# Performance work log

Measured on AMD Instinct MI355X. Metric: run time of the kernel, lower is better.

The kernel has to match this reference:

```python
import jax, jax.numpy as jnp
import numpy as np

KH = KW = 3  # fixed: distortion() generates a 9-tap (3x3) offset grid


def make_offset(h, w, dilation=1.0, skydome=True):
    """Faithful numpy port of DistortionConvLayer.distortion -> [1,h,w,9,2] (last dim = [x_off, y_off])."""
    pi = np.pi
    unit_w = 2.0 * pi / w
    unit_h = pi / (2.0 * h) if skydome else pi / h
    rho = np.tan(unit_w) * dilation
    v = np.array([0.0, 1.0, 0.0])
    r_grid = np.array([[1, -1], [1, 0], [1, 1], [0, -1], [0, 0], [0, 1], [-1, -1], [-1, 0], [-1, 1]], dtype=np.float64)
    xc = int(w * 0.5)
    theta = (xc - 0.5 * w) * unit_w
    y = np.arange(h, dtype=np.float64)
    phi = (h - y) * unit_h if skydome else (h * 0.5 - y) * unit_h  # [h]
    p_u = np.stack([np.cos(phi) * np.cos(theta), np.sin(phi), np.cos(phi) * np.sin(theta)], axis=-1)  # [h,3]
    t_x = np.cross(np.broadcast_to(v, p_u.shape), p_u)  # [h,3]
    t_y = np.cross(p_u, t_x)                            # [h,3]
    # r_sphere: [h,9,3]
    r_sphere = rho * (r_grid[None, :, 0, None] * t_x[:, None, :] + r_grid[None, :, 1, None] * t_y[:, None, :])
    p_ur = p_u[:, None, :] + r_sphere  # [h,9,3]
    ux, uy, uz = p_ur[..., 0], p_ur[..., 1], p_ur[..., 2]
    base = np.arctan2(uz, ux)
    theta_r = np.where(ux > 0, base,
               np.where(ux < 0, np.where(uz >= 0, base + pi, base - pi),
                np.where(uz > 0, pi * 0.5, -pi * 0.5)))
    phi_r = np.arcsin(uy)
    x_r = (theta_r / pi + 1.0) * 0.5 * w
    y_r = (1.0 - 2.0 * phi_r / pi) * h if skydome else (0.5 - phi_r / pi) * h
    k = np.stack([x_r, y_r], axis=-1)          # [h,9,2], entries [x, y] (as in original)
    off = k - k[:, 4:5, :]                      # subtract center tap
    off = np.broadcast_to(off[:, None, :, :], (h, w, 9, 2))  # tile over width
    return off[None].astype(np.float32)         # [1,h,w,9,2]


def setup_inputs() -> dict:
    key = jax.random.key(0)
    k1, k2 = jax.random.split(key)
    B, H, W, C, F = 4, 128, 256, 64, 128
    inputs = jax.random.normal(k1, (B, H, W, C), dtype=jnp.float32)
    fan_in = KH * KW * C
    kernel = jax.random.normal(k2, (fan_in, F), dtype=jnp.float32) * (1.0 / np.sqrt(fan_in))
    bias = jnp.zeros((F,), dtype=jnp.float32)
    return {"inputs": inputs, "kernel": kernel, "bias": bias}


def reference(inputs, kernel, bias):
    B, H, W, C = inputs.shape
    F = kernel.shape[1]
    off = jnp.asarray(make_offset(H, W))  # [1,H,W,9,2], static constant
    # 'same' padding for 3x3, stride 1, dilation 1 -> pad 1 on each side
    xp = jnp.pad(inputs, ((0, 0), (1, 1), (1, 1), (0, 0)))
    in_h, in_w = H + 2, W + 2
    # base conv sampling coordinates (extract_patches order: tap k -> dy=k//3, dx=k%3)
    dy = jnp.repeat(jnp.arange(KH), KW).astype(jnp.float32)  # [9]
    dx = jnp.tile(jnp.arange(KW), KH).astype(jnp.float32)    # [9]
    base_y = jnp.arange(H, dtype=jnp.float32)[None, :, None, None] + dy[None, None, None, :]  # [1,H,1,9]
    base_x = jnp.arange(W, dtype=jnp.float32)[None, None, :, None] + dx[None, None, None, :]  # [1,1,W,9]
    # NOTE: faithful to original: channel 0 of offset (x_r diffs) is added to y, channel 1 to x
    y = base_y + off[..., 0]  # [1,H,W,9]
    x = base_x + off[..., 1]
    y = jnp.clip(y, 0.0, in_h - 1)
    x = jnp.where(x < 0, x + in_w, x)
    x = jnp.where(x > in_w - 1, x - in_w, x)
    y0 = jnp.floor(y).astype(jnp.int32)
    x0 = jnp.floor(x).astype(jnp.int32)
    y1, x1 = y0 + 1, x0 + 1
    y0 = jnp.clip(y0, 0, in_h - 1); y1 = jnp.clip(y1, 0, in_h - 1)
    x0 = jnp.clip(x0, 0, in_w - 1); x1 = jnp.clip(x1, 0, in_w - 1)
    bidx = jnp.arange(B)[:, None, None, None]  # [B,1,1,1], broadcasts against [1,H,W,9]
    gather = lambda yi, xi: xp[bidx, yi, xi]   # -> [B,H,W,9,C]
    p0 = gather(y0, x0); p1 = gather(y0, x1); p2 = gather(y1, x0); p3 = gather(y1, x1)
    y0f, y1f = y0.astype(jnp.float32), y1.astype(jnp.float32)
    x0f, x1f = x0.astype(jnp.float32), x1.astype(jnp.float32)
    w0 = ((y1f - y) * (x1f - x))[..., None]
    w1 = ((y1f - y) * (x - x0f))[..., None]
    w2 = ((y - y0f) * (x1f - x))[..., None]
    w3 = ((y - y0f) * (x - x0f))[..., None]
    pixels = w0 * p0 + w1 * p1 + w2 * p2 + w3 * p3  # [B,H,W,9,C]
    pixels = pixels.reshape(B, H * W, KH * KW * C)
    out = pixels @ kernel + bias                    # [B,HW,F]
    return jax.nn.relu(out.reshape(B, H, W, F))
```

## Files before the change

kernel.cpp:

```cpp
#include <hip/hip_runtime.h>
#include <math.h>

#define Bb 4
#define Hh 128
#define Ww 256
#define Cc 64
#define Ff 128
#define INH 130
#define INW 258

#define WSLOT 72
#define WCOLS 132

typedef __attribute__((ext_vector_type(8))) __bf16 bf16x8;
typedef __attribute__((ext_vector_type(4))) float floatx4;

__device__ __forceinline__ unsigned short f2bf(float f) {
  unsigned int u = __float_as_uint(f);
  unsigned int r = u + 0x7fffu + ((u >> 16) & 1u);
  return (unsigned short)(r >> 16);
}

__global__ void prep_kernel(const float* __restrict__ kmat,
                            float* __restrict__ offtab,
                            unsigned short* __restrict__ kT) {
  int gid = blockIdx.x * 256 + threadIdx.x;
  if (gid < 576 * 128) {
    int f = gid & 127;
    int k = gid >> 7;
    kT[f * 576 + k] = f2bf(kmat[gid]);
  }
  if (gid < Hh * 9) {
    int h = gid / 9;
    int j = gid - h * 9;
    const double pi = 3.14159265358979323846;
    double unit_w = 2.0 * pi / (double)Ww;
    double unit_h = pi / (2.0 * (double)Hh);
    double rho = tan(unit_w);
    double theta = ((double)(Ww / 2) - 0.5 * (double)Ww) * unit_w;
    double phi = ((double)Hh - (double)h) * unit_h;
    double cph = cos(phi), sph = sin(phi);
    double cth = cos(theta), sth = sin(theta);
    double pux = cph * cth, puy = sph, puz = cph * sth;
    double txx = puz, txy = 0.0, txz = -pux;
    double tyx = puy * txz - puz * txy;
    double tyy = puz * txx - pux * txz;
    double tyz = pux * txy - puy * txx;
    const int r0t[9] = {1, 1, 1, 0, 0, 0, -1, -1, -1};
    const int r1t[9] = {-1, 0, 1, -1, 0, 1, -1, 0, 1};
    auto proj = [&](int r0, int r1, double& xr, double& yr) {
      double ux = pux + rho * ((double)r0 * txx + (double)r1 * tyx);
      double uy = puy + rho * ((double)r0 * txy + (double)r1 * tyy);
      double uz = puz + rho * ((double)r0 * txz + (double)r1 * tyz);
      double base = atan2(uz, ux);
      double th;
      if (ux > 0.0)        th = base;
      else if (ux < 0.0)   th = (uz >= 0.0) ? base + pi : base - pi;
      else                 th = (uz > 0.0) ? pi * 0.5 : -pi * 0.5;
      double ph = asin(uy);
      xr = (th / pi + 1.0) * 0.5 * (double)Ww;
      yr = (1.0 - 2.0 * ph / pi) * (double)Hh;
    };
    double xc, yc, xj, yj;
    proj(0, 0, xc, yc);
    proj(r0t[j], r1t[j], xj, yj);
    offtab[gid * 2 + 0] = (float)(xj - xc);
    offtab[gid * 2 + 1] = (float)(yj - yc);
  }
}

__global__ __launch_bounds__(256, 4) void fused_kernel(
    const float* __restrict__ in, const float* __restrict__ bias,
    const unsigned short* __restrict__ kT, const float* __restrict__ offtab,
    float* __restrict__ out) {
  __shared__ unsigned short winH[WCOLS * WSLOT];
  __shared__ unsigned short lB[128 * WSLOT];

  int lidx = ((blockIdx.x & 7) << 7) | (blockIdx.x >> 3);
  int wt = lidx & 1;
  int h  = (lidx >> 1) & 127;
  int b  = lidx >> 8;
  int w0 = wt << 7;

  int tid  = threadIdx.x;
  int lane = tid & 63;
  int wave = tid >> 6;
  int m_base = (wave >> 1) << 6;
  int n_base = (wave & 1) << 6;
  int l15  = lane & 15;
  int quad = lane >> 4;

  floatx4 acc[4][4];
#pragma unroll
  for (int i = 0; i < 4; i++)
#pragma unroll
    for (int j = 0; j < 4; j++) acc[i][j] = (floatx4){0.f, 0.f, 0.f, 0.f};

  const float* inb = in + (size_t)b * Hh * Ww * Cc;

  for (int tap = 0; tap < 9; tap++) {
    float off0 = offtab[(h * 9 + tap) * 2 + 0];
    float off1 = offtab[(h * 9 + tap) * 2 + 1];
    float dyk = (float)(tap / 3), dxk = (float)(tap % 3);

    float y = (float)h + dyk + off0;
    y = fminf(fmaxf(y, 0.f), (float)(INH - 1));
    int y0i = (int)floorf(y);
    int y1i = y0i + 1;
    y0i = min(max(y0i, 0), INH - 1);
    y1i = min(max(y1i, 0), INH - 1);
    float wy0 = (float)y1i - y;
    float wy1 = y - (float)y0i;
    if (!(y0i >= 1 && y0i <= Hh)) wy0 = 0.f;
    if (!(y1i >= 1 && y1i <= Hh)) wy1 = 0.f;
    const float* row0 = inb + (size_t)min(max(y0i - 1, 0), Hh - 1) * Ww * Cc;
    const float* row1 = inb + (size_t)min(max(y1i - 1, 0), Hh - 1) * Ww * Cc;

    float xrep = (float)w0 + dxk + off1;
    float flo  = floorf(xrep);
    int jb = (int)flo - 1;
    float fr = xrep - flo;
    float q00 = wy0 * (1.f - fr), q01 = wy0 * fr;
    float q10 = wy1 * (1.f - fr), q11 = wy1 * fr;

    int slotv[4];
#pragma unroll
    for (int mi = 0; mi < 4; mi++) {
      int w = m_base + mi * 16 + l15;
      float x = (float)(w0 + w) + dxk + off1;
      if (x < 0.f) x += (float)INW;
      if (x > (float)(INW - 1)) x -= (float)INW;
      int x0i = (int)floorf(x);
      int s = x0i - jb;
      if (s < 0) s += INW;
      if (s > 131) s = 131;
      slotv[mi] = s;
    }

#pragma unroll 3
    for (int it = 0; it < 9; it++) {
      int task = tid + (it << 8);
      if (task < WCOLS * 16) {
        int j  = task >> 4;
        int c4 = (task & 15) << 2;
        int col = jb + j;
        if (col < 0) col += INW;
        if (col > INW - 1) col -= INW;
        int ncol = jb + j + 1;
        if (ncol < 0) ncol += INW;
        if (ncol > INW - 1) ncol -= INW;
        bool cok = (col >= 1) & (col <= Ww) & (j < 131);
        bool nok = (ncol >= 1) & (ncol <= Ww) & (j < 131);
        int ci = min(max(col - 1, 0), Ww - 1);
        int ni = min(max(ncol - 1, 0), Ww - 1);
        float4 a0 = *(const float4*)(row0 + ci * Cc + c4);
        float4 a1 = *(const float4*)(row0 + ni * Cc + c4);
        float4 b0 = *(const float4*)(row1 + ci * Cc + c4);
        float4 b1 = *(const float4*)(row1 + ni * Cc + c4);
        float m0 = cok ? 1.f : 0.f, m1 = nok ? 1.f : 0.f;
        float w00 = q00 * m0, w01 = q01 * m1, w10 = q10 * m0, w11 = q11 * m1;
        float4 p;
        p.x = w00 * a0.x + w01 * a1.x + w10 * b0.x + w11 * b1.x;
        p.y = w00 * a0.y + w01 * a1.y + w10 * b0.y + w11 * b1.y;
        p.z = w00 * a0.z + w01 * a1.z + w10 * b0.z + w11 * b1.z;
        p.w = w00 * a0.w + w01 * a1.w + w10 * b0.w + w11 * b1.w;
        uint2 st;
        st.x = (unsigned int)f2bf(p.x) | ((unsigned int)f2bf(p.y) << 16);
        st.y = (unsigned int)f2bf(p.z) | ((unsigned int)f2bf(p.w) << 16);
        *(uint2*)(&winH[j * WSLOT + c4]) = st;
      }
    }

    {
      int f = tid >> 1, seg = tid & 1;
      const unsigned short* src = kT + f * 576 + tap * 64 + seg * 32;
      unsigned short* dst = &lB[f * WSLOT + seg * 32];
#pragma unroll
      for (int i = 0; i < 4; i++)
        *(uint4*)(dst + i * 8) = *(const uint4*)(src + i * 8);
    }

    __syncthreads();

#pragma unroll
    for (int kk = 0; kk < 2; kk++) {
      bf16x8 afrag[4], bfrag[4];
#pragma unroll
      for (int mi = 0; mi < 4; mi++)
        afrag[mi] = *(const bf16x8*)&winH[slotv[mi] * WSLOT + kk * 32 + quad * 8];
#pragma unroll
      for (int ni = 0; ni < 4; ni++)
        bfrag[ni] = *(const bf16x8*)&lB[(n_base + ni * 16 + l15) * WSLOT + kk * 32 + quad * 8];
#pragma unroll
      for (int mi = 0; mi < 4; mi++)
#pragma unroll
        for (int ni = 0; ni < 4; ni++)
          acc[mi][ni] = __builtin_amdgcn_mfma_f32_16x16x32_bf16(
              afrag[mi], bfrag[ni], acc[mi][ni], 0, 0, 0);
    }
    __syncthreads();
  }

  size_t outbase = ((size_t)(b * Hh + h) * Ww + w0);
#pragma unroll
  for (int ni = 0; ni < 4; ni++) {
    int f = n_base + ni * 16 + l15;
    float bv = bias[f];
#pragma unroll
    for (int mi = 0; mi < 4; mi++) {
#pragma unroll
      for (int r = 0; r < 4; r++) {
        int m = m_base + mi * 16 + quad * 4 + r;
        out[(outbase + m) * Ff + f] = fmaxf(acc[mi][ni][r] + bv, 0.f);
      }
    }
  }
}

extern "C" void kernel_launch(void* const* d_in, const int* in_sizes, int n_in,
                              void* d_out, int out_size, void* d_ws, size_t ws_size,
                              hipStream_t stream) {
  const float* in   = (const float*)d_in[0];
  const float* kmat = (const float*)d_in[1];
  const float* bias = (const float*)d_in[2];
  float* out = (float*)d_out;

  float* offtab = (float*)d_ws;
  unsigned short* kT = (unsigned short*)((char*)d_ws + Hh * 9 * 2 * sizeof(float));
  if (ws_size < (size_t)(Hh * 9 * 2 * sizeof(float) + 128 * 576 * sizeof(unsigned short)))
    return;

  prep_kernel<<<288, 256, 0, stream>>>(kmat, offtab, kT);
  fused_kernel<<<Bb * Hh * (Ww / 128), 256, 0, stream>>>(in, bias, kT, offtab, out);
}
```

Measured before the change: 154.8 us.

## Double-buffer LDS window, load weights directly into registers in fragment layout

Weights are pre-permuted into MFMA fragment order so each wave reads its B fragments straight from global memory, which removes the LDS weight tile and its copy. The sampled window is double-buffered by tap parity, so the second barrier per tap is dropped. Each thread now handles 8 channels with wider LDS stores and packs to bf16 with a hardware pack instruction instead of manual rounding. The costs are more global-load traffic for B fragments through L2 and higher register pressure.

```diff
diff --git a/kernel.cpp b/kernel.cpp
--- a/kernel.cpp
+++ b/kernel.cpp
@@ -21,14 +21,26 @@
   return (unsigned short)(r >> 16);
 }
 
+__device__ __forceinline__ unsigned int cvt_pk_bf16(float lo, float hi) {
+  unsigned int r;
+  asm("v_cvt_pk_bf16_f32 %0, %1, %2" : "=v"(r) : "v"(lo), "v"(hi));
+  return r;
+}
+
 __global__ void prep_kernel(const float* __restrict__ kmat,
                             float* __restrict__ offtab,
-                            unsigned short* __restrict__ kT) {
+                            unsigned short* __restrict__ kTB) {
   int gid = blockIdx.x * 256 + threadIdx.x;
   if (gid < 576 * 128) {
     int f = gid & 127;
     int k = gid >> 7;
-    kT[f * 576 + k] = f2bf(kmat[gid]);
+    int tap = k >> 6;
+    int r = k & 63;
+    int kk = r >> 5;
+    int quad = (r >> 3) & 3;
+    int i = r & 7;
+    int chunk = tap * 8 + kk * 4 + quad;
+    kTB[((size_t)chunk * 128 + f) * 8 + i] = f2bf(kmat[gid]);
   }
   if (gid < Hh * 9) {
     int h = gid / 9;
@@ -71,10 +83,9 @@
 
 __global__ __launch_bounds__(256, 4) void fused_kernel(
     const float* __restrict__ in, const float* __restrict__ bias,
-    const unsigned short* __restrict__ kT, const float* __restrict__ offtab,
+    const unsigned short* __restrict__ kTB, const float* __restrict__ offtab,
     float* __restrict__ out) {
-  __shared__ unsigned short winH[WCOLS * WSLOT];
-  __shared__ unsigned short lB[128 * WSLOT];
+  __shared__ unsigned short winH[2][WCOLS * WSLOT];
 
   int lidx = ((blockIdx.x & 7) << 7) | (blockIdx.x >> 3);
   int wt = lidx & 1;
@@ -97,6 +108,7 @@
     for (int j = 0; j < 4; j++) acc[i][j] = (floatx4){0.f, 0.f, 0.f, 0.f};
 
   const float* inb = in + (size_t)b * Hh * Ww * Cc;
+  const bf16x8* kbase = (const bf16x8*)kTB;
 
   for (int tap = 0; tap < 9; tap++) {
     float off0 = offtab[(h * 9 + tap) * 2 + 0];
@@ -137,12 +149,13 @@
       slotv[mi] = s;
     }
 
-#pragma unroll 3
-    for (int it = 0; it < 9; it++) {
+    unsigned short* win = winH[tap & 1];
+
+    for (int it = 0; it < 5; it++) {
       int task = tid + (it << 8);
-      if (task < WCOLS * 16) {
-        int j  = task >> 4;
-        int c4 = (task & 15) << 2;
+      if (task < WCOLS * 8) {
+        int j  = task >> 3;
+        int c8 = (task & 7) << 3;
         int col = jb + j;
         if (col < 0) col += INW;
         if (col > INW - 1) col -= INW;
@@ -153,52 +166,72 @@
         bool nok = (ncol >= 1) & (ncol <= Ww) & (j < 131);
         int ci = min(max(col - 1, 0), Ww - 1);
         int ni = min(max(ncol - 1, 0), Ww - 1);
-        float4 a0 = *(const float4*)(row0 + ci * Cc + c4);
-        float4 a1 = *(const float4*)(row0 + ni * Cc + c4);
-        float4 b0 = *(const float4*)(row1 + ci * Cc + c4);
-        float4 b1 = *(const float4*)(row1 + ni * Cc + c4);
         float m0 = cok ? 1.f : 0.f, m1 = nok ? 1.f : 0.f;
         float w00 = q00 * m0, w01 = q01 * m1, w10 = q10 * m0, w11 = q11 * m1;
-        float4 p;
-        p.x = w00 * a0.x + w01 * a1.x + w10 * b0.x + w11 * b1.x;
-        p.y = w00 * a0.y + w01 * a1.y + w10 * b0.y + w11 * b1.y;
-        p.z = w00 * a0.z + w01 * a1.z + w10 * b0.z + w11 * b1.z;
-        p.w = w00 * a0.w + w01 * a1.w + w10 * b0.w + w11 * b1.w;
-        uint2 st;
-        st.x = (unsigned int)f2bf(p.x) | ((unsigned int)f2bf(p.y) << 16);
-        st.y = (unsigned int)f2bf(p.z) | ((unsigned int)f2bf(p.w) << 16);
-        *(uint2*)(&winH[j * WSLOT + c4]) = st;
+        const float* pa = row0 + ci * Cc + c8;
+        const float* pb = row0 + ni * Cc + c8;
+        const float* pc = row1 + ci * Cc + c8;
+        const float* pd = row1 + ni * Cc + c8;
+        uint4 st;
+        {
+          float4 a0 = *(const float4*)pa;
+          float4 a1 = *(const float4*)pb;
+          float4 b0 = *(const float4*)pc;
+          float4 b1 = *(const float4*)pd;
+          float px = w00 * a0.x + w01 * a1.x + w10 * b0.x + w11 * b1.x;
+          float py = w00 * a0.y + w01 * a1.y + w10 * b0.y + w11 * b1.y;
+          float pz = w00 * a0.z + w01 * a1.z + w10 * b0.z + w11 * b1.z;
+          float pw = w00 * a0.w + w01 * a1.w + w10 * b0.w + w11 * b1.w;
+          st.x = cvt_pk_bf16(px, py);
+          st.y = cvt_pk_bf16(pz, pw);
+        }
+        {
+          float4 a0 = *(const float4*)(pa + 4);
+          float4 a1 = *(const float4*)(pb + 4);
+          float4 b0 = *(const float4*)(pc + 4);
+          float4 b1 = *(const float4*)(pd + 4);
+          float px = w00 * a0.x + w01 * a1.x + w10 * b0.x + w11 * b1.x;
+          float py = w00 * a0.y + w01 * a1.y + w10 * b0.y + w11 * b1.y;
+          float pz = w00 * a0.z + w01 * a1.z + w10 * b0.z + w11 * b1.z;
+          float pw = w00 * a0.w + w01 * a1.w + w10 * b0.w + w11 * b1.w;
+          st.z = cvt_pk_bf16(px, py);
+          st.w = cvt_pk_bf16(pz, pw);
+        }
+        *(uint4*)(&win[j * WSLOT + c8]) = st;
       }
     }
 
-    {
-      int f = tid >> 1, seg = tid & 1;
-      const unsigned short* src = kT + f * 576 + tap * 64 + seg * 32;
-      unsigned short* dst = &lB[f * WSLOT + seg * 32];
-#pragma unroll
-      for (int i = 0; i < 4; i++)
-        *(uint4*)(dst + i * 8) = *(const uint4*)(src + i * 8);
-    }
+    int ch0 = (tap * 8 + quad) * 128;
+    bf16x8 bfrag0[4];
+#pragma unroll
+    for (int v = 0; v < 4; v++)
+      bfrag0[v] = kbase[ch0 + n_base + v * 16 + l15];
 
     __syncthreads();
 
-#pragma unroll
-    for (int kk = 0; kk < 2; kk++) {
-      bf16x8 afrag[4], bfrag[4];
-#pragma unroll
-      for (int mi = 0; mi < 4; mi++)
-        afrag[mi] = *(const bf16x8*)&winH[slotv[mi] * WSLOT + kk * 32 + quad * 8];
-#pragma unroll
-      for (int ni = 0; ni < 4; ni++)
-        bfrag[ni] = *(const bf16x8*)&lB[(n_base + ni * 16 + l15) * WSLOT + kk * 32 + quad * 8];
-#pragma unroll
-      for (int mi = 0; mi < 4; mi++)
-#pragma unroll
-        for (int ni = 0; ni < 4; ni++)
-          acc[mi][ni] = __builtin_amdgcn_mfma_f32_16x16x32_bf16(
-              afrag[mi], bfrag[ni], acc[mi][ni], 0, 0, 0);
-    }
-    __syncthreads();
+    bf16x8 af[4];
+#pragma unroll
+    for (int mi = 0; mi < 4; mi++)
+      af[mi] = *(const bf16x8*)&win[slotv[mi] * WSLOT + quad * 8];
+    bf16x8 bfrag1[4];
+#pragma unroll
+    for (int v = 0; v < 4; v++)
+      bfrag1[v] = kbase[ch0 + 4 * 128 + n_base + v * 16 + l15];
+#pragma unroll
+    for (int mi = 0; mi < 4; mi++)
+#pragma unroll
+      for (int v = 0; v < 4; v++)
+        acc[mi][v] = __builtin_amdgcn_mfma_f32_16x16x32_bf16(
+            af[mi], bfrag0[v], acc[mi][v], 0, 0, 0);
+#pragma unroll
+    for (int mi = 0; mi < 4; mi++)
+      af[mi] = *(const bf16x8*)&win[slotv[mi] * WSLOT + 32 + quad * 8];
+#pragma unroll
+    for (int mi = 0; mi < 4; mi++)
+#pragma unroll
+      for (int v = 0; v < 4; v++)
+        acc[mi][v] = __builtin_amdgcn_mfma_f32_16x16x32_bf16(
+            af[mi], bfrag1[v], acc[mi][v], 0, 0, 0);
   }
 
   size_t outbase = ((size_t)(b * Hh + h) * Ww + w0);
@@ -226,10 +259,10 @@
   float* out = (float*)d_out;
 
   float* offtab = (float*)d_ws;
-  unsigned short* kT = (unsigned short*)((char*)d_ws + Hh * 9 * 2 * sizeof(float));
+  unsigned short* kTB = (unsigned short*)((char*)d_ws + Hh * 9 * 2 * sizeof(float));
   if (ws_size < (size_t)(Hh * 9 * 2 * sizeof(float) + 128 * 576 * sizeof(unsigned short)))
     return;
 
-  prep_kernel<<<288, 256, 0, stream>>>(kmat, offtab, kT);
-  fused_kernel<<<Bb * Hh * (Ww / 128), 256, 0, stream>>>(in, bias, kT, offtab, out);
-}
+  prep_kernel<<<288, 256, 0, stream>>>(kmat, offtab, kTB);
+  fused_kernel<<<Bb * Hh * (Ww / 128), 256, 0, stream>>>(in, bias, kTB, offtab, out);
+}
```

Measured after the change: 146.1 us. 5.6% less time.

## Drop LDS staging; gather bilinear A-fragments and pre-swizzled B directly into registers

Applied to the files above, without the earlier changes.

Removes the shared-memory window and weight staging along with both per-tap barriers. Each lane now gathers its own bilinear samples from global memory, converts them to bf16 with the packed cvt instruction, and feeds MFMA directly. Weights are pre-swizzled into MFMA fragment order in the prep kernel, so B fragments come straight from global/L2. The wave tiling changes to 32 rows by 128 features, and launch bounds drop to 3 blocks per CU. The trade is redundant global/L2 traffic, since each wave re-reads all weights and neighbouring input columns, plus higher register pressure.

```diff
diff --git a/kernel.cpp b/kernel.cpp
--- a/kernel.cpp
+++ b/kernel.cpp
@@ -9,9 +9,6 @@
 #define INH 130
 #define INW 258
 
-#define WSLOT 72
-#define WCOLS 132
-
 typedef __attribute__((ext_vector_type(8))) __bf16 bf16x8;
 typedef __attribute__((ext_vector_type(4))) float floatx4;
 
@@ -21,14 +18,26 @@
   return (unsigned short)(r >> 16);
 }
 
+__device__ __forceinline__ unsigned int cvt_pk_bf16(float lo, float hi) {
+  unsigned int r;
+  asm("v_cvt_pk_bf16_f32 %0, %1, %2" : "=v"(r) : "v"(lo), "v"(hi));
+  return r;
+}
+
 __global__ void prep_kernel(const float* __restrict__ kmat,
                             float* __restrict__ offtab,
-                            unsigned short* __restrict__ kT) {
+                            unsigned short* __restrict__ kTB) {
   int gid = blockIdx.x * 256 + threadIdx.x;
   if (gid < 576 * 128) {
     int f = gid & 127;
     int k = gid >> 7;
-    kT[f * 576 + k] = f2bf(kmat[gid]);
+    int tap = k >> 6;
+    int r = k & 63;
+    int kk = r >> 5;
+    int quad = (r >> 3) & 3;
+    int i = r & 7;
+    int chunk = tap * 8 + kk * 4 + quad;
+    kTB[((size_t)chunk * 128 + f) * 8 + i] = f2bf(kmat[gid]);
   }
   if (gid < Hh * 9) {
     int h = gid / 9;
@@ -69,13 +78,10 @@
   }
 }
 
-__global__ __launch_bounds__(256, 4) void fused_kernel(
+__global__ __launch_bounds__(256, 3) void fused_kernel(
     const float* __restrict__ in, const float* __restrict__ bias,
-    const unsigned short* __restrict__ kT, const float* __restrict__ offtab,
+    const unsigned short* __restrict__ kTB, const float* __restrict__ offtab,
     float* __restrict__ out) {
-  __shared__ unsigned short winH[WCOLS * WSLOT];
-  __shared__ unsigned short lB[128 * WSLOT];
-
   int lidx = ((blockIdx.x & 7) << 7) | (blockIdx.x >> 3);
   int wt = lidx & 1;
   int h  = (lidx >> 1) & 127;
@@ -85,18 +91,18 @@
   int tid  = threadIdx.x;
   int lane = tid & 63;
   int wave = tid >> 6;
-  int m_base = (wave >> 1) << 6;
-  int n_base = (wave & 1) << 6;
+  int m_base = wave << 5;
   int l15  = lane & 15;
   int quad = lane >> 4;
 
-  floatx4 acc[4][4];
-#pragma unroll
-  for (int i = 0; i < 4; i++)
-#pragma unroll
-    for (int j = 0; j < 4; j++) acc[i][j] = (floatx4){0.f, 0.f, 0.f, 0.f};
+  floatx4 acc[2][8];
+#pragma unroll
+  for (int i = 0; i < 2; i++)
+#pragma unroll
+    for (int j = 0; j < 8; j++) acc[i][j] = (floatx4){0.f, 0.f, 0.f, 0.f};
 
   const float* inb = in + (size_t)b * Hh * Ww * Cc;
+  const bf16x8* kbase = (const bf16x8*)kTB;
 
   for (int tap = 0; tap < 9; tap++) {
     float off0 = offtab[(h * 9 + tap) * 2 + 0];
@@ -113,101 +119,84 @@
     float wy1 = y - (float)y0i;
     if (!(y0i >= 1 && y0i <= Hh)) wy0 = 0.f;
     if (!(y1i >= 1 && y1i <= Hh)) wy1 = 0.f;
-    const float* row0 = inb + (size_t)min(max(y0i - 1, 0), Hh - 1) * Ww * Cc;
-    const float* row1 = inb + (size_t)min(max(y1i - 1, 0), Hh - 1) * Ww * Cc;
+    const char* r0 = (const char*)(inb + (size_t)min(max(y0i - 1, 0), Hh - 1) * Ww * Cc);
+    const char* r1 = (const char*)(inb + (size_t)min(max(y1i - 1, 0), Hh - 1) * Ww * Cc);
 
     float xrep = (float)w0 + dxk + off1;
-    float flo  = floorf(xrep);
-    int jb = (int)flo - 1;
-    float fr = xrep - flo;
+    float fr = xrep - floorf(xrep);
     float q00 = wy0 * (1.f - fr), q01 = wy0 * fr;
     float q10 = wy1 * (1.f - fr), q11 = wy1 * fr;
 
-    int slotv[4];
-#pragma unroll
-    for (int mi = 0; mi < 4; mi++) {
-      int w = m_base + mi * 16 + l15;
-      float x = (float)(w0 + w) + dxk + off1;
+    int offc[2], offn[2];
+    float w00[2], w01[2], w10[2], w11[2];
+#pragma unroll
+    for (int mi = 0; mi < 2; mi++) {
+      int wout = m_base + mi * 16 + l15;
+      float x = (float)(w0 + wout) + dxk + off1;
       if (x < 0.f) x += (float)INW;
       if (x > (float)(INW - 1)) x -= (float)INW;
-      int x0i = (int)floorf(x);
-      int s = x0i - jb;
-      if (s < 0) s += INW;
-      if (s > 131) s = 131;
-      slotv[mi] = s;
+      int c0 = (int)floorf(x);
+      int c1 = min(c0 + 1, INW - 1);
+      bool m0 = (unsigned)(c0 - 1) < (unsigned)Ww;
+      bool m1 = (unsigned)(c1 - 1) < (unsigned)Ww;
+      offc[mi] = (((c0 - 1) & (Ww - 1)) << 8) + (quad << 5);
+      offn[mi] = (((c1 - 1) & (Ww - 1)) << 8) + (quad << 5);
+      w00[mi] = m0 ? q00 : 0.f;
+      w01[mi] = m1 ? q01 : 0.f;
+      w10[mi] = m0 ? q10 : 0.f;
+      w11[mi] = m1 ? q11 : 0.f;
     }
 
-#pragma unroll 3
-    for (int it = 0; it < 9; it++) {
-      int task = tid + (it << 8);
-      if (task < WCOLS * 16) {
-        int j  = task >> 4;
-        int c4 = (task & 15) << 2;
-        int col = jb + j;
-        if (col < 0) col += INW;
-        if (col > INW - 1) col -= INW;
-        int ncol = jb + j + 1;
-        if (ncol < 0) ncol += INW;
-        if (ncol > INW - 1) ncol -= INW;
-        bool cok = (col >= 1) & (col <= Ww) & (j < 131);
-        bool nok = (ncol >= 1) & (ncol <= Ww) & (j < 131);
-        int ci = min(max(col - 1, 0), Ww - 1);
-        int ni = min(max(ncol - 1, 0), Ww - 1);
-        float4 a0 = *(const float4*)(row0 + ci * Cc + c4);
-        float4 a1 = *(const float4*)(row0 + ni * Cc + c4);
-        float4 b0 = *(const float4*)(row1 + ci * Cc + c4);
-        float4 b1 = *(const float4*)(row1 + ni * Cc + c4);
-        float m0 = cok ? 1.f : 0.f, m1 = nok ? 1.f : 0.f;
-        float w00 = q00 * m0, w01 = q01 * m1, w10 = q10 * m0, w11 = q11 * m1;
-        float4 p;
-        p.x = w00 * a0.x + w01 * a1.x + w10 * b0.x + w11 * b1.x;
-        p.y = w00 * a0.y + w01 * a1.y + w10 * b0.y + w11 * b1.y;
-        p.z = w00 * a0.z + w01 * a1.z + w10 * b0.z + w11 * b1.z;
-        p.w = w00 * a0.w + w01 * a1.w + w10 * b0.w + w11 * b1.w;
-        uint2 st;
-        st.x = (unsigned int)f2bf(p.x) | ((unsigned int)f2bf(p.y) << 16);
-        st.y = (unsigned int)f2bf(p.z) | ((unsigned int)f2bf(p.w) << 16);
-        *(uint2*)(&winH[j * WSLOT + c4]) = st;
+#pragma unroll
+    for (int kk = 0; kk < 2; kk++) {
+      int ch0 = (tap * 8 + kk * 4 + quad) * 128;
+      bf16x8 bfrag[8];
+#pragma unroll
+      for (int ni = 0; ni < 8; ni++)
+        bfrag[ni] = kbase[ch0 + ni * 16 + l15];
+
+#pragma unroll
+      for (int mi = 0; mi < 2; mi++) {
+        int oc = offc[mi] + kk * 128;
+        int on = offn[mi] + kk * 128;
+        float4 a0l = *(const float4*)(r0 + oc);
+        float4 a0h = *(const float4*)(r0 + oc + 16);
+        float4 a1l = *(const float4*)(r0 + on);
+        float4 a1h = *(const float4*)(r0 + on + 16);
+        float4 b0l = *(const float4*)(r1 + oc);
+        float4 b0h = *(const float4*)(r1 + oc + 16);
+        float4 b1l = *(const float4*)(r1 + on);
+        float4 b1h = *(const float4*)(r1 + on + 16);
+        float W00 = w00[mi], W01 = w01[mi], W10 = w10[mi], W11 = w11[mi];
+        float p0 = W00 * a0l.x + W01 * a1l.x + W10 * b0l.x + W11 * b1l.x;
+        float p1 = W00 * a0l.y + W01 * a1l.y + W10 * b0l.y + W11 * b1l.y;
+        float p2 = W00 * a0l.z + W01 * a1l.z + W10 * b0l.z + W11 * b1l.z;
+        float p3 = W00 * a0l.w + W01 * a1l.w + W10 * b0l.w + W11 * b1l.w;
+        float p4 = W00 * a0h.x + W01 * a1h.x + W10 * b0h.x + W11 * b1h.x;
+        float p5 = W00 * a0h.y + W01 * a1h.y + W10 * b0h.y + W11 * b1h.y;
+        float p6 = W00 * a0h.z + W01 * a1h.z + W10 * b0h.z + W11 * b1h.z;
+        float p7 = W00 * a0h.w + W01 * a1h.w + W10 * b0h.w + W11 * b1h.w;
+        union { uint4 u; bf16x8 v; } afc;
+        afc.u.x = cvt_pk_bf16(p0, p1);
+        afc.u.y = cvt_pk_bf16(p2, p3);
+        afc.u.z = cvt_pk_bf16(p4, p5);
+        afc.u.w = cvt_pk_bf16(p6, p7);
+        bf16x8 af = afc.v;
+#pragma unroll
+        for (int ni = 0; ni < 8; ni++)
+          acc[mi][ni] = __builtin_amdgcn_mfma_f32_16x16x32_bf16(
+              af, bfrag[ni], acc[mi][ni], 0, 0, 0);
       }
     }
-
-    {
-      int f = tid >> 1, seg = tid & 1;
-      const unsigned short* src = kT + f * 576 + tap * 64 + seg * 32;
-      unsigned short* dst = &lB[f * WSLOT + seg * 32];
-#pragma unroll
-      for (int i = 0; i < 4; i++)
-        *(uint4*)(dst + i * 8) = *(const uint4*)(src + i * 8);
-    }
-
-    __syncthreads();
-
-#pragma unroll
-    for (int kk = 0; kk < 2; kk++) {
-      bf16x8 afrag[4], bfrag[4];
-#pragma unroll
-      for (int mi = 0; mi < 4; mi++)
-        afrag[mi] = *(const bf16x8*)&winH[slotv[mi] * WSLOT + kk * 32 + quad * 8];
-#pragma unroll
-      for (int ni = 0; ni < 4; ni++)
-        bfrag[ni] = *(const bf16x8*)&lB[(n_base + ni * 16 + l15) * WSLOT + kk * 32 + quad * 8];
-#pragma unroll
-      for (int mi = 0; mi < 4; mi++)
-#pragma unroll
-        for (int ni = 0; ni < 4; ni++)
-          acc[mi][ni] = __builtin_amdgcn_mfma_f32_16x16x32_bf16(
-              afrag[mi], bfrag[ni], acc[mi][ni], 0, 0, 0);
-    }
-    __syncthreads();
   }
 
   size_t outbase = ((size_t)(b * Hh + h) * Ww + w0);
 #pragma unroll
-  for (int ni = 0; ni < 4; ni++) {
-    int f = n_base + ni * 16 + l15;
+  for (int ni = 0; ni < 8; ni++) {
+    int f = ni * 16 + l15;
     float bv = bias[f];
 #pragma unroll
-    for (int mi = 0; mi < 4; mi++) {
+    for (int mi = 0; mi < 2; mi++) {
 #pragma unroll
       for (int r = 0; r < 4; r++) {
         int m = m_base + mi * 16 + quad * 4 + r;
@@ -226,10 +215,10 @@
   float* out = (float*)d_out;
 
   float* offtab = (float*)d_ws;
-  unsigned short* kT = (unsigned short*)((char*)d_ws + Hh * 9 * 2 * sizeof(float));
+  unsigned short* kTB = (unsigned short*)((char*)d_ws + Hh * 9 * 2 * sizeof(float));
   if (ws_size < (size_t)(Hh * 9 * 2 * sizeof(float) + 128 * 576 * sizeof(unsigned short)))
     return;
 
-  prep_kernel<<<288, 256, 0, stream>>>(kmat, offtab, kT);
-  fused_kernel<<<Bb * Hh * (Ww / 128), 256, 0, stream>>>(in, bias, kT, offtab, out);
-}
+  prep_kernel<<<288, 256, 0, stream>>>(kmat, offtab, kTB);
+  fused_kernel<<<Bb * Hh * (Ww / 128), 256, 0, stream>>>(in, bias, kTB, offtab, out);
+}
```

After: 271.5 us. +75.4%, slower.
